# Kernel optimization log

Measured on AMD Instinct MI355X. Metric: run time of the kernel, lower is better.

The kernel has to match this reference:

```python
import jax, jax.numpy as jnp
import numpy as np

HIDDEN = 1024
NUM_HEADS = 16
HEAD_DIM = HIDDEN // NUM_HEADS


def setup_inputs() -> dict:
    key = jax.random.key(0)
    ks = jax.random.split(key, 9)
    B, S, Hs = 2, 2048, HIDDEN
    scale = 1.0 / np.sqrt(Hs)
    inp = {
        "hidden_state": jax.random.normal(ks[0], (B, S, Hs), dtype=jnp.float32),
        # causal mask, exactly (B, num_heads, S, S) as the module's assert requires
        "attention_mask": jnp.broadcast_to(
            jnp.tril(jnp.ones((S, S), dtype=bool)), (B, NUM_HEADS, S, S)
        ),
        "wq": jax.random.normal(ks[1], (Hs, Hs), dtype=jnp.float32) * scale,
        "bq": jnp.zeros((Hs,), dtype=jnp.float32),
        "wk": jax.random.normal(ks[2], (Hs, Hs), dtype=jnp.float32) * scale,
        "bk": jnp.zeros((Hs,), dtype=jnp.float32),
        "wv": jax.random.normal(ks[3], (Hs, Hs), dtype=jnp.float32) * scale,
        "bv": jnp.zeros((Hs,), dtype=jnp.float32),
        "wo": jax.random.normal(ks[4], (Hs, Hs), dtype=jnp.float32) * scale,
        "bo": jnp.zeros((Hs,), dtype=jnp.float32),
    }
    return inp


def _split_heads(x):
    B, S, _ = x.shape
    return x.reshape(B, S, NUM_HEADS, HEAD_DIM).transpose(0, 2, 1, 3)  # (B,H,S,D)


def reference(hidden_state, attention_mask, wq, bq, wk, bk, wv, bv, wo, bo):
    B, S, Hs = hidden_state.shape
    # torch nn.Linear: x @ W.T + b
    q = _split_heads(hidden_state @ wq.T + bq)
    k = _split_heads(hidden_state @ wk.T + bk)
    v = _split_heads(hidden_state @ wv.T + bv)
    scores = jnp.einsum("bhsd,bhtd->bhst", q, k) / jnp.sqrt(
        jnp.asarray(HEAD_DIM, dtype=jnp.float32)
    )
    scores = jnp.where(attention_mask, scores, -jnp.inf)
    probs = jax.nn.softmax(scores, axis=-1)
    # dropout p=0.0 (eval/deterministic) -> identity
    out = jnp.einsum("bhst,bhtd->bhsd", probs, v)
    out = out.transpose(0, 2, 1, 3).reshape(B, S, Hs)
    return out @ wo.T + bo
```

## Files before the change

kernel.cpp:

```cpp
#include <hip/hip_runtime.h>
#include <stdint.h>
#include <stddef.h>


typedef __attribute__((ext_vector_type(8))) short short8;
typedef __attribute__((ext_vector_type(4))) float f32x4;
typedef __attribute__((ext_vector_type(4))) unsigned int u32x4;
typedef __attribute__((ext_vector_type(2))) unsigned int u32x2;
typedef __attribute__((ext_vector_type(4))) unsigned short u16x4;

static __device__ __forceinline__ unsigned short f2bf(float f){
  union { float f; unsigned u; } v; v.f = f;
  unsigned r = v.u + 0x7FFFu + ((v.u >> 16) & 1u);
  return (unsigned short)(r >> 16);
}
static __device__ __forceinline__ unsigned pk2bf(float lo, float hi){
  return (unsigned)f2bf(lo) | ((unsigned)f2bf(hi) << 16);
}

static __device__ __forceinline__ void gl_lds16(const void* g, void* l){
  __builtin_amdgcn_global_load_lds((const __attribute__((address_space(1))) void*)g,
                                   (__attribute__((address_space(3))) void*)l, 16, 0, 0);
}

__global__ __launch_bounds__(256) void k_cvt_all(const float* __restrict__ X,
                                                 const float* __restrict__ w0, const float* __restrict__ w1,
                                                 const float* __restrict__ w2, const float* __restrict__ w3,
                                                 unsigned short* __restrict__ Xb,
                                                 unsigned short* __restrict__ Wb){
  int bid = blockIdx.x;
  const float* src; unsigned short* dst; int i;
  if (bid < 4096){ src = X; dst = Xb; i = bid*256 + threadIdx.x; }
  else {
    int w = (bid - 4096) >> 10;
    const float* srcs[4] = {w0,w1,w2,w3};
    src = srcs[w]; dst = Wb + (size_t)w*1048576u;
    i = ((bid - 4096) & 1023)*256 + threadIdx.x;
  }
  f32x4 x = ((const f32x4*)src)[i];
  u16x4 y = { f2bf(x[0]), f2bf(x[1]), f2bf(x[2]), f2bf(x[3]) };
  ((u16x4*)dst)[i] = y;
}

template<int MODE, int MT>
__global__ __launch_bounds__(256) void k_gemm_bt(
    const unsigned short* __restrict__ A,
    const unsigned short* __restrict__ B,
    const float* __restrict__ bias0, const float* __restrict__ bias1, const float* __restrict__ bias2,
    void* __restrict__ Cout, int N, int K)
{
  static_assert(MT==64 || MT==128, "MT");
  constexpr int I  = MT/32;
  constexpr int NA = MT/64;
  __shared__ unsigned short lds_a[MT*32];
  __shared__ unsigned short lds_b[128*32];
  const int t = threadIdx.x;
  const int lane = t & 63, wave = t >> 6;
  const int wy = wave >> 1, wx = wave & 1;
  const int m0 = blockIdx.y * MT, n0 = blockIdx.x * 128;
  const int mrow = lane & 15, quad = lane >> 4;
  const unsigned short* ga = A + (size_t)(m0 + (t>>2)) * K + (t&3)*8;
  const unsigned short* gb = B + (size_t)(n0 + (t>>2)) * K + (t&3)*8;
  char* la = (char*)lds_a + wave*1024;
  char* lb = (char*)lds_b + wave*1024;

  f32x4 acc[I][4];
  #pragma unroll
  for (int i=0;i<I;i++)
    #pragma unroll
    for (int j=0;j<4;j++) acc[i][j] = (f32x4){0.f,0.f,0.f,0.f};

  for (int k0=0;k0<K;k0+=32){
    __syncthreads();
    #pragma unroll
    for (int p=0;p<NA;p++) gl_lds16(ga + (size_t)p*64*K + k0, la + p*4096);
    #pragma unroll
    for (int p=0;p<2;p++)  gl_lds16(gb + (size_t)p*64*K + k0, lb + p*4096);
    __syncthreads();
    short8 af[I], bf[4];
    #pragma unroll
    for (int i=0;i<I;i++) af[i] = *(const short8*)(lds_a + (wy*(MT/2)+i*16+mrow)*32 + quad*8);
    #pragma unroll
    for (int j=0;j<4;j++) bf[j] = *(const short8*)(lds_b + (wx*64+j*16+mrow)*32 + quad*8);
    #pragma unroll
    for (int i=0;i<I;i++)
      #pragma unroll
      for (int j=0;j<4;j++)
        acc[i][j] = __builtin_amdgcn_mfma_f32_16x16x32_bf16(af[i], bf[j], acc[i][j], 0,0,0);
  }

  #pragma unroll
  for (int j=0;j<4;j++){
    int col = n0 + wx*64 + j*16 + mrow;
    float bv;
    if (MODE==0){
      int cb = col >> 10;
      const float* bp = (cb==0)?bias0:((cb==1)?bias1:bias2);
      bv = bp[col & 1023];
    } else {
      bv = bias0[col];
    }
    #pragma unroll
    for (int i=0;i<I;i++){
      int rbase = m0 + wy*(MT/2) + i*16 + quad*4;
      #pragma unroll
      for (int r=0;r<4;r++){
        float v = acc[i][j][r] + bv;
        if (MODE==1) ((float*)Cout)[(size_t)(rbase+r)*N + col] = v;
        else         ((unsigned short*)Cout)[(size_t)(rbase+r)*N + col] = f2bf(v);
      }
    }
  }
}

__global__ __launch_bounds__(256) void k_vt(const unsigned short* __restrict__ QKV,
                                            unsigned short* __restrict__ Vt){
  __shared__ unsigned short tile[64][72];
  const int bh = blockIdx.y, b = bh >> 4, h = bh & 15;
  const int s0 = blockIdx.x * 64;
  const unsigned short* vp = QKV + (size_t)b*2048*3072 + 2048 + (size_t)h*64;
  const int r = threadIdx.x >> 3, c = (threadIdx.x & 7) * 8;
  #pragma unroll
  for (int p=0;p<2;p++){
    int s = r + p*32;
    *(u32x4*)&tile[s][c] = *(const u32x4*)(vp + (size_t)(s0+s)*3072 + c);
  }
  __syncthreads();
  unsigned short* op = Vt + (size_t)bh*64*2048;
  #pragma unroll
  for (int p=0;p<2;p++){
    int d = r + p*32;
    union { short8 v; unsigned short u[8]; } o;
    #pragma unroll
    for (int i=0;i<8;i++) o.u[i] = tile[c+i][d];
    *(short8*)(op + (size_t)d*2048 + s0 + c) = o.v;
  }
}

__global__ __launch_bounds__(256) void k_attn(const unsigned short* __restrict__ QKV,
                                              const unsigned short* __restrict__ Vt,
                                              unsigned short* __restrict__ Ctx){
  __shared__ unsigned short lds_k[64*72];
  __shared__ unsigned short lds_v[64*72];
  __shared__ unsigned short lds_p[4][16*72];
  const int t = threadIdx.x;
  const int lane = t & 63, wave = t >> 6;
  const int mrow = lane & 15, quad = lane >> 4;
  const int bh = blockIdx.y, b = bh >> 4, h = bh & 15;
  const int qt = (bh & 16) ? (15 - blockIdx.x) : blockIdx.x;
  const int q0 = qt * 128;
  const size_t qkvbase = (size_t)b*2048*3072 + (size_t)h*64;

  short8 qf[2][2];
  #pragma unroll
  for (int qh=0;qh<2;qh++){
    const unsigned short* qp = QKV + qkvbase + (size_t)(q0 + qh*64 + wave*16 + mrow) * 3072;
    qf[qh][0] = *(const short8*)(qp + quad*8);
    qf[qh][1] = *(const short8*)(qp + 32 + quad*8);
  }
  float l_i[2] = {0.f, 0.f};
  f32x4 oacc[2][4];
  #pragma unroll
  for (int qh=0;qh<2;qh++)
    #pragma unroll
    for (int c=0;c<4;c++) oacc[qh][c] = (f32x4){0.f,0.f,0.f,0.f};

  const int njt = 2*qt + 2;
  const unsigned short* kbase = QKV + qkvbase + 1024;
  const unsigned short* vbase = Vt + (size_t)bh*64*2048;
  const int sr = t >> 3, sc = (t & 7) * 8;

  for (int jt=0;jt<njt;jt++){
    const int j0 = jt*64;
    __syncthreads();
    #pragma unroll
    for (int p=0;p<2;p++){
      int r = sr + p*32;
      *(u32x4*)(lds_k + r*72 + sc) = *(const u32x4*)(kbase + (size_t)(j0+r)*3072 + sc);
      *(u32x4*)(lds_v + r*72 + sc) = *(const u32x4*)(vbase + (size_t)r*2048 + j0 + sc);
    }
    __syncthreads();

    #pragma unroll
    for (int qh=0;qh<2;qh++){
      if (qh==0 && jt==njt-1) continue;
      const int grow = q0 + qh*64 + wave*16 + mrow;

      f32x4 sacc[4];
      #pragma unroll
      for (int jb=0;jb<4;jb++) sacc[jb] = (f32x4){0.f,0.f,0.f,0.f};
      #pragma unroll
      for (int jb=0;jb<4;jb++)
        #pragma unroll
        for (int kk=0;kk<2;kk++){
          short8 kf = *(const short8*)(lds_k + (jb*16+mrow)*72 + kk*32 + quad*8);
          sacc[jb] = __builtin_amdgcn_mfma_f32_16x16x32_bf16(kf, qf[qh][kk], sacc[jb], 0,0,0);
        }

      float s[4][4];
      if (jt == 2*qt + qh){
        #pragma unroll
        for (int jb=0;jb<4;jb++){
          int jg = j0 + jb*16 + quad*4;
          #pragma unroll
          for (int r=0;r<4;r++){
            float v = fmaf(sacc[jb][r], 0.125f, -16.f);
            s[jb][r] = __expf((jg + r <= grow) ? v : -1e30f);
          }
        }
      } else {
        #pragma unroll
        for (int jb=0;jb<4;jb++)
          #pragma unroll
          for (int r=0;r<4;r++)
            s[jb][r] = __expf(fmaf(sacc[jb][r], 0.125f, -16.f));
      }
      #pragma unroll
      for (int jb=0;jb<4;jb++)
        #pragma unroll
        for (int r=0;r<4;r++) l_i[qh] += s[jb][r];

      unsigned short* pp = lds_p[wave];
      #pragma unroll
      for (int jb=0;jb<4;jb++){
        u32x2 w = { pk2bf(s[jb][0], s[jb][1]), pk2bf(s[jb][2], s[jb][3]) };
        *(u32x2*)(pp + mrow*72 + jb*16 + quad*4) = w;
      }
      __asm__ volatile("s_waitcnt lgkmcnt(0)" ::: "memory");
      short8 pf[2];
      pf[0] = *(const short8*)(pp + mrow*72 + quad*8);
      pf[1] = *(const short8*)(pp + mrow*72 + 32 + quad*8);

      #pragma unroll
      for (int c=0;c<4;c++)
        #pragma unroll
        for (int kk=0;kk<2;kk++){
          short8 vf = *(const short8*)(lds_v + (c*16+mrow)*72 + kk*32 + quad*8);
          oacc[qh][c] = __builtin_amdgcn_mfma_f32_16x16x32_bf16(vf, pf[kk], oacc[qh][c], 0,0,0);
        }
    }
  }

  unsigned short* cp = Ctx + (size_t)b*2048*1024 + (size_t)h*64;
  #pragma unroll
  for (int qh=0;qh<2;qh++){
    float l = l_i[qh];
    l += __shfl_xor(l, 16);
    l += __shfl_xor(l, 32);
    float rl = 1.f / l;
    size_t rowoff = (size_t)(q0 + qh*64 + wave*16 + mrow) * 1024;
    #pragma unroll
    for (int c=0;c<4;c++){
      u32x2 w = { pk2bf(oacc[qh][c][0]*rl, oacc[qh][c][1]*rl),
                  pk2bf(oacc[qh][c][2]*rl, oacc[qh][c][3]*rl) };
      *(u32x2*)(cp + rowoff + c*16 + quad*4) = w;
    }
  }
}

extern "C" void kernel_launch(void* const* d_in, const int* in_sizes, int n_in,
                              void* d_out, int out_size, void* d_ws, size_t ws_size,
                              hipStream_t stream){
  const float* X  = (const float*)d_in[0];
  const float* wq = (const float*)d_in[2];
  const float* bq = (const float*)d_in[3];
  const float* wk = (const float*)d_in[4];
  const float* bk = (const float*)d_in[5];
  const float* wv = (const float*)d_in[6];
  const float* bv = (const float*)d_in[7];
  const float* wo = (const float*)d_in[8];
  const float* bo = (const float*)d_in[9];

  char* ws = (char*)d_ws;
  unsigned short* Xb   = (unsigned short*)(ws);
  unsigned short* Wb   = (unsigned short*)(ws + (8u<<20));
  unsigned short* QKVb = (unsigned short*)(ws + (16u<<20));
  unsigned short* Vt   = (unsigned short*)(ws + (40u<<20));
  unsigned short* Ctxb = (unsigned short*)(ws + (48u<<20));

  k_cvt_all<<<dim3(8192), 256, 0, stream>>>(X, wq, wk, wv, wo, Xb, Wb);
  k_gemm_bt<0,128><<<dim3(24, 32), 256, 0, stream>>>(Xb, Wb, bq, bk, bv, QKVb, 3072, 1024);
  k_vt  <<<dim3(32, 32), 256, 0, stream>>>(QKVb, Vt);
  k_attn<<<dim3(16, 32), 256, 0, stream>>>(QKVb, Vt, Ctxb);
  k_gemm_bt<1,64><<<dim3(8, 64), 256, 0, stream>>>(Ctxb, Wb + 3u*1048576u, bo, bo, bo,
                                                   d_out, 1024, 1024);
}
```

Baseline: 717.4 us.

## Fuse V transpose into QKV GEMM epilogue and use exp2 in softmax

The QKV projection GEMM now writes the V columns straight into the transposed per-head Vt layout from its epilogue, so the separate transpose kernel and its extra read and write of V are removed. The attention kernel folds log2(e) into the score scale and offset and calls the hardware exp2 intrinsic in place of __expf. The fused epilogue writes 8-byte chunks strided by 2048 elements, so its stores are less coalesced than the row-major path. It also leaves a dead unused temporary in place.

```diff
diff --git a/kernel.cpp b/kernel.cpp
--- a/kernel.cpp
+++ b/kernel.cpp
@@ -47,7 +47,7 @@
     const unsigned short* __restrict__ A,
     const unsigned short* __restrict__ B,
     const float* __restrict__ bias0, const float* __restrict__ bias1, const float* __restrict__ bias2,
-    void* __restrict__ Cout, int N, int K)
+    void* __restrict__ Cout, unsigned short* __restrict__ Vt, int N, int K)
 {
   static_assert(MT==64 || MT==128, "MT");
   constexpr int I  = MT/32;
@@ -89,6 +89,7 @@
         acc[i][j] = __builtin_amdgcn_mfma_f32_16x16x32_bf16(af[i], bf[j], acc[i][j], 0,0,0);
   }
 
+  const bool vblk = (MODE==0) && (n0 >= 2048);
   #pragma unroll
   for (int j=0;j<4;j++){
     int col = n0 + wx*64 + j*16 + mrow;
@@ -103,37 +104,23 @@
     #pragma unroll
     for (int i=0;i<I;i++){
       int rbase = m0 + wy*(MT/2) + i*16 + quad*4;
-      #pragma unroll
-      for (int r=0;r<4;r++){
-        float v = acc[i][j][r] + bv;
-        if (MODE==1) ((float*)Cout)[(size_t)(rbase+r)*N + col] = v;
-        else         ((unsigned short*)Cout)[(size_t)(rbase+r)*N + col] = f2bf(v);
+      if (vblk){
+        int bh = (rbase >> 11) * 16 + ((col >> 6) & 15);
+        unsigned short* vp = Vt + ((size_t)bh*64 + (col & 63))*2048 + (rbase & 2047);
+        u32x2 w = { pk2bf(acc[i][0 ][0], 0.f) };
+        (void)w;
+        u32x2 wv = { pk2bf(acc[i][j][0]+bv, acc[i][j][1]+bv),
+                     pk2bf(acc[i][j][2]+bv, acc[i][j][3]+bv) };
+        *(u32x2*)vp = wv;
+      } else {
+        #pragma unroll
+        for (int r=0;r<4;r++){
+          float v = acc[i][j][r] + bv;
+          if (MODE==1) ((float*)Cout)[(size_t)(rbase+r)*N + col] = v;
+          else         ((unsigned short*)Cout)[(size_t)(rbase+r)*N + col] = f2bf(v);
+        }
       }
     }
-  }
-}
-
-__global__ __launch_bounds__(256) void k_vt(const unsigned short* __restrict__ QKV,
-                                            unsigned short* __restrict__ Vt){
-  __shared__ unsigned short tile[64][72];
-  const int bh = blockIdx.y, b = bh >> 4, h = bh & 15;
-  const int s0 = blockIdx.x * 64;
-  const unsigned short* vp = QKV + (size_t)b*2048*3072 + 2048 + (size_t)h*64;
-  const int r = threadIdx.x >> 3, c = (threadIdx.x & 7) * 8;
-  #pragma unroll
-  for (int p=0;p<2;p++){
-    int s = r + p*32;
-    *(u32x4*)&tile[s][c] = *(const u32x4*)(vp + (size_t)(s0+s)*3072 + c);
-  }
-  __syncthreads();
-  unsigned short* op = Vt + (size_t)bh*64*2048;
-  #pragma unroll
-  for (int p=0;p<2;p++){
-    int d = r + p*32;
-    union { short8 v; unsigned short u[8]; } o;
-    #pragma unroll
-    for (int i=0;i<8;i++) o.u[i] = tile[c+i][d];
-    *(short8*)(op + (size_t)d*2048 + s0 + c) = o.v;
   }
 }
 
@@ -150,6 +137,8 @@
   const int qt = (bh & 16) ? (15 - blockIdx.x) : blockIdx.x;
   const int q0 = qt * 128;
   const size_t qkvbase = (size_t)b*2048*3072 + (size_t)h*64;
+  const float C1 = 0.125f * 1.44269504f;
+  const float C0 = -16.f  * 1.44269504f;
 
   short8 qf[2][2];
   #pragma unroll
@@ -204,8 +193,8 @@
           int jg = j0 + jb*16 + quad*4;
           #pragma unroll
           for (int r=0;r<4;r++){
-            float v = fmaf(sacc[jb][r], 0.125f, -16.f);
-            s[jb][r] = __expf((jg + r <= grow) ? v : -1e30f);
+            float v = fmaf(sacc[jb][r], C1, C0);
+            s[jb][r] = __builtin_amdgcn_exp2f((jg + r <= grow) ? v : -1e30f);
           }
         }
       } else {
@@ -213,7 +202,7 @@
         for (int jb=0;jb<4;jb++)
           #pragma unroll
           for (int r=0;r<4;r++)
-            s[jb][r] = __expf(fmaf(sacc[jb][r], 0.125f, -16.f));
+            s[jb][r] = __builtin_amdgcn_exp2f(fmaf(sacc[jb][r], C1, C0));
       }
       #pragma unroll
       for (int jb=0;jb<4;jb++)
@@ -279,9 +268,8 @@
   unsigned short* Ctxb = (unsigned short*)(ws + (48u<<20));
 
   k_cvt_all<<<dim3(8192), 256, 0, stream>>>(X, wq, wk, wv, wo, Xb, Wb);
-  k_gemm_bt<0,128><<<dim3(24, 32), 256, 0, stream>>>(Xb, Wb, bq, bk, bv, QKVb, 3072, 1024);
-  k_vt  <<<dim3(32, 32), 256, 0, stream>>>(QKVb, Vt);
+  k_gemm_bt<0,128><<<dim3(24, 32), 256, 0, stream>>>(Xb, Wb, bq, bk, bv, QKVb, Vt, 3072, 1024);
   k_attn<<<dim3(16, 32), 256, 0, stream>>>(QKVb, Vt, Ctxb);
   k_gemm_bt<1,64><<<dim3(8, 64), 256, 0, stream>>>(Ctxb, Wb + 3u*1048576u, bo, bo, bo,
-                                                   d_out, 1024, 1024);
-}
+                                                   d_out, nullptr, 1024, 1024);
+}
```

Result: no change. 715.5 us (-0.3%).
